# Performance work log

Hardware: AMD Instinct MI355X
Metric: run time of the kernel (lower is better)

Reference implementation:

```python
import jax, jax.numpy as jnp
import numpy as np

NUM_HEADS = 16

def setup_inputs() -> dict:
    key = jax.random.key(0)
    ks = jax.random.split(key, 9)
    E = 1024
    T, B = 2048, 2
    s = E ** -0.5
    return {
        "query": jax.random.normal(ks[0], (T, B, E), dtype=jnp.float32),
        "Wq": jax.random.normal(ks[1], (E, E), dtype=jnp.float32) * s,
        "bq": jax.random.normal(ks[2], (E,), dtype=jnp.float32) * 0.02,
        "Wk": jax.random.normal(ks[3], (E, E), dtype=jnp.float32) * s,
        "bk": jax.random.normal(ks[4], (E,), dtype=jnp.float32) * 0.02,
        "Wv": jax.random.normal(ks[5], (E, E), dtype=jnp.float32) * s,
        "bv": jax.random.normal(ks[6], (E,), dtype=jnp.float32) * 0.02,
        "Wo": jax.random.normal(ks[7], (E, E), dtype=jnp.float32) * s,
        "bo": jax.random.normal(ks[8], (E,), dtype=jnp.float32) * 0.02,
    }

def reference(query, Wq, bq, Wk, bk, Wv, bv, Wo, bo):
    # query: [T, B, E] (seq-first, fairseq/ESM layout)
    T, B, E = query.shape
    H = NUM_HEADS
    D = E // H
    scaling = D ** -0.5
    # projections (eqx Linear: x @ W.T + b); note k/v also come from `query` (self-attention)
    q = (query @ Wq.T + bq) * scaling
    k = query @ Wk.T + bk
    v = query @ Wv.T + bv
    # [T, B, E] -> [B*H, T, D]
    q = q.reshape(T, B * H, D).transpose(1, 0, 2)
    k = k.reshape(T, B * H, D).transpose(1, 0, 2)
    v = v.reshape(T, B * H, D).transpose(1, 0, 2)
    # full score matrix [B*H, T, T], softmax in fp32 (as in original)
    scores = jnp.einsum('ntd,nsd->nts', q, k)
    attn_w = jax.nn.softmax(scores.astype(jnp.float32), axis=-1)
    attn = jnp.einsum('nts,nsd->ntd', attn_w.astype(v.dtype), v)
    # [B*H, T, D] -> [T, B, E]
    attn = attn.transpose(1, 0, 2).reshape(T, B, E)
    return attn @ Wo.T + bo
```

## Files before the change

### kernel.cpp

```cpp
#include <hip/hip_runtime.h>
#include <hip/hip_bf16.h>


typedef __attribute__((ext_vector_type(8))) short short8;
typedef __attribute__((ext_vector_type(4))) float f32x4;
typedef __attribute__((ext_vector_type(16))) float f32x16;
typedef __attribute__((ext_vector_type(4))) unsigned u32x4;

#define T_DIM 2048
#define B_DIM 2
#define E_DIM 1024
#define H_DIM 16
#define D_DIM 64
#define M_ROWS (T_DIM * B_DIM)
#define QKV_N (3 * E_DIM)
#define HEAD_ELEMS (32 * 2048 * 64)
#define LOG2E 1.44269504088896340736f

__device__ __forceinline__ unsigned short f2bf(float f) {
    unsigned u = __builtin_bit_cast(unsigned, f);
    unsigned r = (u + 0x7fffu + ((u >> 16) & 1u)) >> 16;
    return (unsigned short)r;
}

__device__ __forceinline__ float bf2f(unsigned short s) {
    unsigned u = ((unsigned)s) << 16;
    return __builtin_bit_cast(float, u);
}

__device__ __forceinline__ unsigned cvt_pk_bf16(float lo, float hi) {
    unsigned d;
    asm("v_cvt_pk_bf16_f32 %0, %1, %2" : "=v"(d) : "v"(lo), "v"(hi));
    return d;
}

__device__ __forceinline__ void gload_lds16(const void* g, void* l) {
    __builtin_amdgcn_global_load_lds(
        (const __attribute__((address_space(1))) void*)g,
        (__attribute__((address_space(3))) void*)l, 16, 0, 0);
}

__device__ __forceinline__ f32x16 mfma32(short8 a, short8 b, f32x16 c) {
    return __builtin_amdgcn_mfma_f32_32x32x16_bf16(a, b, c, 0, 0, 0);
}

__global__ __launch_bounds__(256) void cast_all(
    const float* __restrict__ X,
    const float* __restrict__ Wq, const float* __restrict__ Wk,
    const float* __restrict__ Wv, const float* __restrict__ Wo,
    unsigned short* __restrict__ Xbf,
    unsigned short* __restrict__ Wcat,
    unsigned short* __restrict__ Wobf)
{
    int idx = blockIdx.x * 256 + threadIdx.x;
    size_t base = (size_t)idx * 8;
    int row = (int)(base >> 10);
    int col = (int)(base & 1023);
    const float* src;
    unsigned short* dst;
    float scale = 1.0f;
    if (row < 4096) {
        src = X + base;
        dst = Xbf + base;
    } else if (row < 7168) {
        int wrow = row - 4096;
        if (wrow < 1024)      { src = Wq + ((size_t)wrow << 10) + col; scale = 0.125f * LOG2E; }
        else if (wrow < 2048) { src = Wk + ((size_t)(wrow - 1024) << 10) + col; }
        else                  { src = Wv + ((size_t)(wrow - 2048) << 10) + col; }
        dst = Wcat + ((size_t)wrow << 10) + col;
    } else {
        int wrow = row - 7168;
        src = Wo + ((size_t)wrow << 10) + col;
        dst = Wobf + ((size_t)wrow << 10) + col;
    }
    float4 f0 = *(const float4*)src;
    float4 f1 = *(const float4*)(src + 4);
    short8 r;
    r[0] = (short)f2bf(f0.x * scale);
    r[1] = (short)f2bf(f0.y * scale);
    r[2] = (short)f2bf(f0.z * scale);
    r[3] = (short)f2bf(f0.w * scale);
    r[4] = (short)f2bf(f1.x * scale);
    r[5] = (short)f2bf(f1.y * scale);
    r[6] = (short)f2bf(f1.z * scale);
    r[7] = (short)f2bf(f1.w * scale);
    *(short8*)dst = r;
}

__global__ __launch_bounds__(256) void bias_fuse(
    const float* __restrict__ bq, const float* __restrict__ bk,
    const float* __restrict__ bv, float* __restrict__ biasq)
{
    int i = blockIdx.x * 256 + threadIdx.x;
    if (i < 1024)       biasq[i] = 0.125f * LOG2E * bq[i];
    else if (i < 2048)  biasq[i] = bk[i - 1024];
    else if (i < 3072)  biasq[i] = bv[i - 2048];
}

template <int MODE>
__global__ __launch_bounds__(256) void gemm_bt(
    const unsigned short* __restrict__ A,
    const unsigned short* __restrict__ B,
    const float* __restrict__ bias,
    void* __restrict__ outp,
    int M, int N, int K)
{
    __shared__ alignas(16) unsigned short As[2][128 * 32];
    __shared__ alignas(16) unsigned short Bs[2][128 * 32];
    const int tid = threadIdx.x;
    const int wave = tid >> 6, lane = tid & 63;
    const int lr = lane & 15, lg = lane >> 4;
    const int nbx = N >> 7;
    const int bx = blockIdx.x % nbx, by = blockIdx.x / nbx;
    const int wr = wave >> 1, wc = wave & 1;

    f32x4 acc[4][4] = {};

    auto stage = [&](int buf, int kt) {
#pragma unroll
        for (int pass = 0; pass < 2; ++pass) {
            int c = pass * 256 + wave * 64 + lane;
            int row = c >> 2, kc = c & 3;
            gload_lds16(A + (size_t)(by * 128 + row) * K + kt + kc * 8,
                        (char*)&As[buf][0] + c * 16);
            gload_lds16(B + (size_t)(bx * 128 + row) * K + kt + kc * 8,
                        (char*)&Bs[buf][0] + c * 16);
        }
    };

    const int NK = K >> 5;
    stage(0, 0);
    for (int ki = 0; ki < NK; ++ki) {
        const int buf = ki & 1;
        if (ki < NK - 1) {
            stage(buf ^ 1, (ki + 1) * 32);
            asm volatile("s_waitcnt vmcnt(4)" ::: "memory");
        } else {
            asm volatile("s_waitcnt vmcnt(0)" ::: "memory");
        }
        __builtin_amdgcn_s_barrier();
        __builtin_amdgcn_sched_barrier(0);

        short8 af[4], bf[4];
#pragma unroll
        for (int m = 0; m < 4; ++m)
            af[m] = *(const short8*)&As[buf][(wr * 64 + m * 16 + lr) * 32 + lg * 8];
#pragma unroll
        for (int n = 0; n < 4; ++n)
            bf[n] = *(const short8*)&Bs[buf][(wc * 64 + n * 16 + lr) * 32 + lg * 8];
        __builtin_amdgcn_s_setprio(1);
#pragma unroll
        for (int m = 0; m < 4; ++m)
#pragma unroll
            for (int n = 0; n < 4; ++n)
                acc[m][n] = __builtin_amdgcn_mfma_f32_16x16x32_bf16(af[m], bf[n], acc[m][n], 0, 0, 0);
        __builtin_amdgcn_s_setprio(0);

        asm volatile("s_waitcnt lgkmcnt(0)" ::: "memory");
        __builtin_amdgcn_sched_barrier(0);
        __builtin_amdgcn_s_barrier();
    }

    const int gcol0 = bx * 128 + wc * 64;
    const int grow0 = by * 128 + wr * 64;
    if (MODE == 0) {
        unsigned short* qb = (unsigned short*)outp;
#pragma unroll
        for (int m = 0; m < 4; ++m) {
#pragma unroll
            for (int n = 0; n < 4; ++n) {
                int col = gcol0 + n * 16 + lr;
                float bsv = bias[col];
                int which = col >> 10;
                int e = col & 1023;
                int h = e >> 6, d = e & 63;
                if (which < 2) {
                    unsigned short* bufb = qb + (size_t)which * HEAD_ELEMS;
#pragma unroll
                    for (int j = 0; j < 4; ++j) {
                        int r = grow0 + m * 16 + lg * 4 + j;
                        int t = r >> 1, b = r & 1;
                        int bh = b * 16 + h;
                        bufb[((size_t)bh * 2048 + t) * 64 + d] = f2bf(acc[m][n][j] + bsv);
                    }
                } else {
                    unsigned* vT32 = (unsigned*)(qb + (size_t)2 * HEAD_ELEMS);
                    int t0 = (grow0 + m * 16 + lg * 4) >> 1;
                    int dwidx = t0 >> 1;
                    int dwp = (dwidx & ~6) | ((dwidx & 2) << 1) | ((dwidx & 4) >> 1);
                    unsigned w0 = (unsigned)f2bf(acc[m][n][0] + bsv) |
                                  ((unsigned)f2bf(acc[m][n][2] + bsv) << 16);
                    unsigned w1 = (unsigned)f2bf(acc[m][n][1] + bsv) |
                                  ((unsigned)f2bf(acc[m][n][3] + bsv) << 16);
                    vT32[(size_t)(h * 64 + d) * 1024 + dwp] = w0;
                    vT32[(size_t)((16 + h) * 64 + d) * 1024 + dwp] = w1;
                }
            }
        }
    } else {
        float* O = (float*)outp;
#pragma unroll
        for (int m = 0; m < 4; ++m) {
#pragma unroll
            for (int n = 0; n < 4; ++n) {
                int col = gcol0 + n * 16 + lr;
                float bsv = bias[col];
#pragma unroll
                for (int j = 0; j < 4; ++j) {
                    int r = grow0 + m * 16 + lg * 4 + j;
                    O[(size_t)r * N + col] = acc[m][n][j] + bsv;
                }
            }
        }
    }
}

struct AttnCtx {
    const unsigned short* kh;
    const unsigned short* vh;
    int tid, ql, hi;
};

template<bool DO_PV, bool DO_STAGE>
__device__ __forceinline__ void attn_step(
    const AttnCtx& cx, int kt_next,
    const char* Kb, const char* Vprv,
    char* Kst, char* Vst,
    const short8 (&qv)[4],
    const short8 (&paP)[4], short8 (&paC)[4],
    f32x16 (&accO)[2], float& lrun)
{
    const int tid = cx.tid, ql = cx.ql, hi = cx.hi;
    if constexpr (DO_STAGE) {
#pragma unroll
        for (int p = 0; p < 2; ++p) {
            int c = p * 256 + tid;
            int row = c >> 3;
            int sxb = ((c & 7) * 16) ^ ((row & 7) << 4);
            gload_lds16(cx.kh + (size_t)(kt_next + row) * 64 + (sxb >> 1), Kst + c * 16);
        }
#pragma unroll
        for (int p = 0; p < 2; ++p) {
            int c = p * 256 + tid;
            int d = c >> 3;
            int sxb = ((c & 7) * 16) ^ ((d & 7) << 4);
            gload_lds16(cx.vh + (size_t)d * 2048 + kt_next + (sxb >> 1), Vst + c * 16);
        }
        asm volatile("s_waitcnt vmcnt(4)" ::: "memory");
    } else {
        asm volatile("s_waitcnt vmcnt(0)" ::: "memory");
    }
    __builtin_amdgcn_s_barrier();
    __builtin_amdgcn_sched_barrier(0);

    f32x16 st[2] = {};
    __builtin_amdgcn_s_setprio(1);
#pragma unroll
    for (int m = 0; m < 2; ++m) {
        int krow = m * 32 + ql;
#pragma unroll
        for (int c = 0; c < 4; ++c) {
            int bo = (krow * 128 + c * 32 + hi * 16) ^ ((krow & 7) << 4);
            short8 ka = *(const short8*)(Kb + bo);
            st[m] = mfma32(ka, qv[c], st[m]);
        }
    }
    if constexpr (DO_PV) {
#pragma unroll
        for (int n = 0; n < 2; ++n) {
            int d = n * 32 + ql;
#pragma unroll
            for (int kc = 0; kc < 4; ++kc) {
                int bo = (d * 128 + kc * 32 + hi * 16) ^ ((d & 7) << 4);
                short8 va = *(const short8*)(Vprv + bo);
                accO[n] = mfma32(va, paP[kc], accO[n]);
            }
        }
    }
    __builtin_amdgcn_s_setprio(0);
    __builtin_amdgcn_sched_barrier(0);

    float rs0 = 0.f, rs1 = 0.f, rs2 = 0.f, rs3 = 0.f;
#pragma unroll
    for (int m = 0; m < 2; ++m) {
#pragma unroll
        for (int r = 0; r < 16; r += 4) {
            float e0 = __builtin_amdgcn_exp2f(st[m][r + 0]);
            float e1 = __builtin_amdgcn_exp2f(st[m][r + 1]);
            float e2 = __builtin_amdgcn_exp2f(st[m][r + 2]);
            float e3 = __builtin_amdgcn_exp2f(st[m][r + 3]);
            st[m][r + 0] = e0; st[m][r + 1] = e1;
            st[m][r + 2] = e2; st[m][r + 3] = e3;
            rs0 += e0; rs1 += e1; rs2 += e2; rs3 += e3;
        }
    }
    lrun += (rs0 + rs1) + (rs2 + rs3);

#pragma unroll
    for (int kc = 0; kc < 4; ++kc) {
        int m = kc >> 1, b8 = (kc & 1) * 8;
        u32x4 u;
        u[0] = cvt_pk_bf16(st[m][b8 + 0], st[m][b8 + 1]);
        u[1] = cvt_pk_bf16(st[m][b8 + 2], st[m][b8 + 3]);
        u[2] = cvt_pk_bf16(st[m][b8 + 4], st[m][b8 + 5]);
        u[3] = cvt_pk_bf16(st[m][b8 + 6], st[m][b8 + 7]);
        paC[kc] = __builtin_bit_cast(short8, u);
    }

    asm volatile("s_waitcnt lgkmcnt(0)" ::: "memory");
    __builtin_amdgcn_sched_barrier(0);
    __builtin_amdgcn_s_barrier();
}

__global__ __launch_bounds__(256, 4) void attn_fwd(
    const unsigned short* __restrict__ q,
    const unsigned short* __restrict__ k,
    const unsigned short* __restrict__ vT,
    unsigned short* __restrict__ o0,
    unsigned short* __restrict__ o1,
    float* __restrict__ lsum)
{
    __shared__ alignas(16) unsigned short Ks[2][64 * 64];
    __shared__ alignas(16) unsigned short Vs[3][64 * 64];
    const int tid = threadIdx.x, wv = tid >> 6, l = tid & 63;
    const int ql = l & 31, hi = l >> 5;
    const int lid = blockIdx.x;
    const int xcd = lid & 7, slot = lid >> 3;
    const int bh = xcd * 4 + (slot >> 5);
    const int sub = slot & 31;
    const int q0 = (sub >> 1) * 128;
    const int half = sub & 1;
    const int kv0 = half * 1024;
    const unsigned short* qh = q + (size_t)bh * (2048 * 64);
    AttnCtx cx;
    cx.kh = k + (size_t)bh * (2048 * 64);
    cx.vh = vT + (size_t)bh * (64 * 2048);
    cx.tid = tid; cx.ql = ql; cx.hi = hi;

    char* K0 = (char*)&Ks[0][0];
    char* K1 = (char*)&Ks[1][0];
    char* V0 = (char*)&Vs[0][0];
    char* V1 = (char*)&Vs[1][0];
    char* V2 = (char*)&Vs[2][0];
    auto VB = [&](int i) -> char* { return i == 0 ? V0 : (i == 1 ? V1 : V2); };

    const int qrow = q0 + wv * 32 + ql;
    short8 qv[4];
#pragma unroll
    for (int c = 0; c < 4; ++c)
        qv[c] = *(const short8*)&qh[(size_t)qrow * 64 + c * 16 + hi * 8];

    f32x16 accO[2] = {};
    float lrun = 0.0f;
    short8 paA[4], paB[4];

    {
#pragma unroll
        for (int p = 0; p < 2; ++p) {
            int c = p * 256 + tid;
            int row = c >> 3;
            int sxb = ((c & 7) * 16) ^ ((row & 7) << 4);
            gload_lds16(cx.kh + (size_t)(kv0 + row) * 64 + (sxb >> 1), K0 + c * 16);
        }
#pragma unroll
        for (int p = 0; p < 2; ++p) {
            int c = p * 256 + tid;
            int d = c >> 3;
            int sxb = ((c & 7) * 16) ^ ((d & 7) << 4);
            gload_lds16(cx.vh + (size_t)d * 2048 + kv0 + (sxb >> 1), V0 + c * 16);
        }
    }

    int vp = 2, vn = 1;
    int vc = 0;
    auto rot = [&]() { vp = vc; vc = vn; vn = (vn == 2) ? 0 : vn + 1; };

    attn_step<false, true>(cx, kv0 + 64, K0, nullptr, K1, VB(vn), qv, paB, paA, accO, lrun);
    rot();
    for (int t = 1; t < 15; t += 2) {
        attn_step<true, true>(cx, kv0 + (t + 1) * 64, K1, VB(vp), K0, VB(vn),
                              qv, paA, paB, accO, lrun);
        rot();
        attn_step<true, true>(cx, kv0 + (t + 2) * 64, K0, VB(vp), K1, VB(vn),
                              qv, paB, paA, accO, lrun);
        rot();
    }
    attn_step<true, false>(cx, 0, K1, VB(vp), nullptr, nullptr, qv, paA, paB, accO, lrun);
#pragma unroll
    for (int n = 0; n < 2; ++n) {
        int d = n * 32 + ql;
#pragma unroll
        for (int kc = 0; kc < 4; ++kc) {
            int bo = (d * 128 + kc * 32 + hi * 16) ^ ((d & 7) << 4);
            short8 va = *(const short8*)(V0 + bo);
            accO[n] = mfma32(va, paB[kc], accO[n]);
        }
    }

    const float lh = lrun + __shfl_xor(lrun, 32);
    if (hi == 0)
        lsum[half * 65536 + bh * 2048 + qrow] = lh;
    unsigned short* outb = half ? o1 : o0;
    const int b = bh >> 4, h = bh & 15;
    const int orow = qrow * 2 + b;
#pragma unroll
    for (int n = 0; n < 2; ++n)
#pragma unroll
        for (int rq = 0; rq < 4; ++rq) {
            uint2 u;
            u.x = cvt_pk_bf16(accO[n][rq * 4 + 0], accO[n][rq * 4 + 1]);
            u.y = cvt_pk_bf16(accO[n][rq * 4 + 2], accO[n][rq * 4 + 3]);
            *(uint2*)&outb[(size_t)orow * 1024 + h * 64 + n * 32 + rq * 8 + hi * 4] = u;
        }
}

__global__ __launch_bounds__(256) void merge_attn(
    const unsigned short* __restrict__ o1,
    const float* __restrict__ lsum,
    unsigned short* __restrict__ o0)
{
    int idx = blockIdx.x * 256 + threadIdx.x;
    size_t base = (size_t)idx * 8;
    int r = (int)(base >> 10), cb = (int)(base & 1023);
    int t = r >> 1, b = r & 1, h = cb >> 6;
    int bh = b * 16 + h;
    float l0 = lsum[bh * 2048 + t];
    float l1 = lsum[65536 + bh * 2048 + t];
    float inv = 1.0f / (l0 + l1);
    short8 x = *(const short8*)(o0 + base);
    short8 y = *(const short8*)(o1 + base);
    u32x4 u;
#pragma unroll
    for (int j = 0; j < 4; ++j) {
        float f0 = (bf2f((unsigned short)x[2*j])   + bf2f((unsigned short)y[2*j]))   * inv;
        float f1 = (bf2f((unsigned short)x[2*j+1]) + bf2f((unsigned short)y[2*j+1])) * inv;
        u[j] = cvt_pk_bf16(f0, f1);
    }
    *(short8*)(o0 + base) = __builtin_bit_cast(short8, u);
}

extern "C" void kernel_launch(void* const* d_in, const int* in_sizes, int n_in,
                              void* d_out, int out_size, void* d_ws, size_t ws_size,
                              hipStream_t stream) {
    const float* X  = (const float*)d_in[0];
    const float* Wq = (const float*)d_in[1];
    const float* bq = (const float*)d_in[2];
    const float* Wk = (const float*)d_in[3];
    const float* bk = (const float*)d_in[4];
    const float* Wv = (const float*)d_in[5];
    const float* bv = (const float*)d_in[6];
    const float* Wo = (const float*)d_in[7];
    const float* bo = (const float*)d_in[8];
    float* out = (float*)d_out;

    char* ws = (char*)d_ws;
    if (ws_size < ((size_t)49 << 20)) return;
    unsigned short* Xbf   = (unsigned short*)(ws);
    unsigned short* Wcat  = (unsigned short*)(ws + ((size_t)8  << 20));
    unsigned short* Wobf  = (unsigned short*)(ws + ((size_t)14 << 20));
    unsigned short* qb    = (unsigned short*)(ws + ((size_t)16 << 20));
    unsigned short* ab    = (unsigned short*)(ws + ((size_t)40 << 20));
    float*          biasq = (float*)(ws + ((size_t)48 << 20));
    unsigned short* kb  = qb + (size_t)HEAD_ELEMS;
    unsigned short* vTb = qb + (size_t)2 * HEAD_ELEMS;
    unsigned short* o1   = Xbf;
    float*          lsum = (float*)Wcat;

    cast_all<<<4096, 256, 0, stream>>>(X, Wq, Wk, Wv, Wo, Xbf, Wcat, Wobf);
    bias_fuse<<<12, 256, 0, stream>>>(bq, bk, bv, biasq);
    gemm_bt<0><<<dim3((M_ROWS / 128) * (QKV_N / 128)), 256, 0, stream>>>(
        Xbf, Wcat, biasq, (void*)qb, M_ROWS, QKV_N, E_DIM);
    attn_fwd<<<dim3(32 * 16 * 2), 256, 0, stream>>>(qb, kb, vTb, ab, o1, lsum);
    merge_attn<<<2048, 256, 0, stream>>>(o1, lsum, ab);
    gemm_bt<1><<<dim3((M_ROWS / 128) * (E_DIM / 128)), 256, 0, stream>>>(
        ab, Wobf, bo, (void*)out, M_ROWS, E_DIM, E_DIM);
}
```

Measured before the change: 127.6 us.

## Process two query tiles per wave and drop split-KV merge kernel

The attention kernel now gives each wave 64 query rows as two 32-row tiles. Both tiles share the K fragments loaded from LDS and the V reads in the PV step, which halves LDS traffic per query. The KV split into two halves is removed: each block walks the full 2048-key sequence, normalises by the row sum itself and writes the final output. This removes the merge_attn kernel and its partial-output and lsum round trip through memory. In exchange the grid shrinks from 1024 to 256 blocks, launch bounds allow fewer blocks per CU, and register pressure roughly doubles, which can cut occupancy and latency hiding.

```diff
diff --git a/kernel.cpp b/kernel.cpp
--- a/kernel.cpp
+++ b/kernel.cpp
@@ -21,11 +21,6 @@
     unsigned u = __builtin_bit_cast(unsigned, f);
     unsigned r = (u + 0x7fffu + ((u >> 16) & 1u)) >> 16;
     return (unsigned short)r;
-}
-
-__device__ __forceinline__ float bf2f(unsigned short s) {
-    unsigned u = ((unsigned)s) << 16;
-    return __builtin_bit_cast(float, u);
 }
 
 __device__ __forceinline__ unsigned cvt_pk_bf16(float lo, float hi) {
@@ -226,9 +221,11 @@
     const AttnCtx& cx, int kt_next,
     const char* Kb, const char* Vprv,
     char* Kst, char* Vst,
-    const short8 (&qv)[4],
-    const short8 (&paP)[4], short8 (&paC)[4],
-    f32x16 (&accO)[2], float& lrun)
+    const short8 (&qv0)[4], const short8 (&qv1)[4],
+    const short8 (&paP0)[4], const short8 (&paP1)[4],
+    short8 (&paC0)[4], short8 (&paC1)[4],
+    f32x16 (&accO0)[2], f32x16 (&accO1)[2],
+    float& lrun0, float& lrun1)
 {
     const int tid = cx.tid, ql = cx.ql, hi = cx.hi;
     if constexpr (DO_STAGE) {
@@ -253,18 +250,24 @@
     __builtin_amdgcn_s_barrier();
     __builtin_amdgcn_sched_barrier(0);
 
-    f32x16 st[2] = {};
-    __builtin_amdgcn_s_setprio(1);
+    short8 ka[8];
 #pragma unroll
     for (int m = 0; m < 2; ++m) {
         int krow = m * 32 + ql;
 #pragma unroll
         for (int c = 0; c < 4; ++c) {
             int bo = (krow * 128 + c * 32 + hi * 16) ^ ((krow & 7) << 4);
-            short8 ka = *(const short8*)(Kb + bo);
-            st[m] = mfma32(ka, qv[c], st[m]);
-        }
-    }
+            ka[m * 4 + c] = *(const short8*)(Kb + bo);
+        }
+    }
+
+    f32x16 st0[2] = {}, st1[2] = {};
+    __builtin_amdgcn_s_setprio(1);
+#pragma unroll
+    for (int m = 0; m < 2; ++m)
+#pragma unroll
+        for (int c = 0; c < 4; ++c)
+            st0[m] = mfma32(ka[m * 4 + c], qv0[c], st0[m]);
     if constexpr (DO_PV) {
 #pragma unroll
         for (int n = 0; n < 2; ++n) {
@@ -273,38 +276,69 @@
             for (int kc = 0; kc < 4; ++kc) {
                 int bo = (d * 128 + kc * 32 + hi * 16) ^ ((d & 7) << 4);
                 short8 va = *(const short8*)(Vprv + bo);
-                accO[n] = mfma32(va, paP[kc], accO[n]);
-            }
-        }
-    }
+                accO0[n] = mfma32(va, paP0[kc], accO0[n]);
+                accO1[n] = mfma32(va, paP1[kc], accO1[n]);
+            }
+        }
+    }
+#pragma unroll
+    for (int m = 0; m < 2; ++m)
+#pragma unroll
+        for (int c = 0; c < 4; ++c)
+            st1[m] = mfma32(ka[m * 4 + c], qv1[c], st1[m]);
     __builtin_amdgcn_s_setprio(0);
-    __builtin_amdgcn_sched_barrier(0);
-
-    float rs0 = 0.f, rs1 = 0.f, rs2 = 0.f, rs3 = 0.f;
-#pragma unroll
-    for (int m = 0; m < 2; ++m) {
-#pragma unroll
-        for (int r = 0; r < 16; r += 4) {
-            float e0 = __builtin_amdgcn_exp2f(st[m][r + 0]);
-            float e1 = __builtin_amdgcn_exp2f(st[m][r + 1]);
-            float e2 = __builtin_amdgcn_exp2f(st[m][r + 2]);
-            float e3 = __builtin_amdgcn_exp2f(st[m][r + 3]);
-            st[m][r + 0] = e0; st[m][r + 1] = e1;
-            st[m][r + 2] = e2; st[m][r + 3] = e3;
-            rs0 += e0; rs1 += e1; rs2 += e2; rs3 += e3;
-        }
-    }
-    lrun += (rs0 + rs1) + (rs2 + rs3);
-
-#pragma unroll
-    for (int kc = 0; kc < 4; ++kc) {
-        int m = kc >> 1, b8 = (kc & 1) * 8;
-        u32x4 u;
-        u[0] = cvt_pk_bf16(st[m][b8 + 0], st[m][b8 + 1]);
-        u[1] = cvt_pk_bf16(st[m][b8 + 2], st[m][b8 + 3]);
-        u[2] = cvt_pk_bf16(st[m][b8 + 4], st[m][b8 + 5]);
-        u[3] = cvt_pk_bf16(st[m][b8 + 6], st[m][b8 + 7]);
-        paC[kc] = __builtin_bit_cast(short8, u);
+
+    {
+        float rs0 = 0.f, rs1 = 0.f, rs2 = 0.f, rs3 = 0.f;
+#pragma unroll
+        for (int m = 0; m < 2; ++m)
+#pragma unroll
+            for (int r = 0; r < 16; r += 4) {
+                float e0 = __builtin_amdgcn_exp2f(st0[m][r + 0]);
+                float e1 = __builtin_amdgcn_exp2f(st0[m][r + 1]);
+                float e2 = __builtin_amdgcn_exp2f(st0[m][r + 2]);
+                float e3 = __builtin_amdgcn_exp2f(st0[m][r + 3]);
+                st0[m][r + 0] = e0; st0[m][r + 1] = e1;
+                st0[m][r + 2] = e2; st0[m][r + 3] = e3;
+                rs0 += e0; rs1 += e1; rs2 += e2; rs3 += e3;
+            }
+        lrun0 += (rs0 + rs1) + (rs2 + rs3);
+#pragma unroll
+        for (int kc = 0; kc < 4; ++kc) {
+            int m = kc >> 1, b8 = (kc & 1) * 8;
+            u32x4 u;
+            u[0] = cvt_pk_bf16(st0[m][b8 + 0], st0[m][b8 + 1]);
+            u[1] = cvt_pk_bf16(st0[m][b8 + 2], st0[m][b8 + 3]);
+            u[2] = cvt_pk_bf16(st0[m][b8 + 4], st0[m][b8 + 5]);
+            u[3] = cvt_pk_bf16(st0[m][b8 + 6], st0[m][b8 + 7]);
+            paC0[kc] = __builtin_bit_cast(short8, u);
+        }
+    }
+    {
+        float rs0 = 0.f, rs1 = 0.f, rs2 = 0.f, rs3 = 0.f;
+#pragma unroll
+        for (int m = 0; m < 2; ++m)
+#pragma unroll
+            for (int r = 0; r < 16; r += 4) {
+                float e0 = __builtin_amdgcn_exp2f(st1[m][r + 0]);
+                float e1 = __builtin_amdgcn_exp2f(st1[m][r + 1]);
+                float e2 = __builtin_amdgcn_exp2f(st1[m][r + 2]);
+                float e3 = __builtin_amdgcn_exp2f(st1[m][r + 3]);
+                st1[m][r + 0] = e0; st1[m][r + 1] = e1;
+                st1[m][r + 2] = e2; st1[m][r + 3] = e3;
+                rs0 += e0; rs1 += e1; rs2 += e2; rs3 += e3;
+            }
+        lrun1 += (rs0 + rs1) + (rs2 + rs3);
+#pragma unroll
+        for (int kc = 0; kc < 4; ++kc) {
+            int m = kc >> 1, b8 = (kc & 1) * 8;
+            u32x4 u;
+            u[0] = cvt_pk_bf16(st1[m][b8 + 0], st1[m][b8 + 1]);
+            u[1] = cvt_pk_bf16(st1[m][b8 + 2], st1[m][b8 + 3]);
+            u[2] = cvt_pk_bf16(st1[m][b8 + 4], st1[m][b8 + 5]);
+            u[3] = cvt_pk_bf16(st1[m][b8 + 6], st1[m][b8 + 7]);
+            paC1[kc] = __builtin_bit_cast(short8, u);
+        }
     }
 
     asm volatile("s_waitcnt lgkmcnt(0)" ::: "memory");
@@ -312,13 +346,11 @@
     __builtin_amdgcn_s_barrier();
 }
 
-__global__ __launch_bounds__(256, 4) void attn_fwd(
+__global__ __launch_bounds__(256, 2) void attn_fwd(
     const unsigned short* __restrict__ q,
     const unsigned short* __restrict__ k,
     const unsigned short* __restrict__ vT,
-    unsigned short* __restrict__ o0,
-    unsigned short* __restrict__ o1,
-    float* __restrict__ lsum)
+    unsigned short* __restrict__ outb)
 {
     __shared__ alignas(16) unsigned short Ks[2][64 * 64];
     __shared__ alignas(16) unsigned short Vs[3][64 * 64];
@@ -326,11 +358,8 @@
     const int ql = l & 31, hi = l >> 5;
     const int lid = blockIdx.x;
     const int xcd = lid & 7, slot = lid >> 3;
-    const int bh = xcd * 4 + (slot >> 5);
-    const int sub = slot & 31;
-    const int q0 = (sub >> 1) * 128;
-    const int half = sub & 1;
-    const int kv0 = half * 1024;
+    const int bh = xcd * 4 + (slot >> 3);
+    const int q0 = (slot & 7) * 256;
     const unsigned short* qh = q + (size_t)bh * (2048 * 64);
     AttnCtx cx;
     cx.kh = k + (size_t)bh * (2048 * 64);
@@ -344,15 +373,17 @@
     char* V2 = (char*)&Vs[2][0];
     auto VB = [&](int i) -> char* { return i == 0 ? V0 : (i == 1 ? V1 : V2); };
 
-    const int qrow = q0 + wv * 32 + ql;
-    short8 qv[4];
-#pragma unroll
-    for (int c = 0; c < 4; ++c)
-        qv[c] = *(const short8*)&qh[(size_t)qrow * 64 + c * 16 + hi * 8];
-
-    f32x16 accO[2] = {};
-    float lrun = 0.0f;
-    short8 paA[4], paB[4];
+    const int qrow0 = q0 + wv * 64 + ql;
+    short8 qv0[4], qv1[4];
+#pragma unroll
+    for (int c = 0; c < 4; ++c) {
+        qv0[c] = *(const short8*)&qh[(size_t)qrow0 * 64 + c * 16 + hi * 8];
+        qv1[c] = *(const short8*)&qh[(size_t)(qrow0 + 32) * 64 + c * 16 + hi * 8];
+    }
+
+    f32x16 accO0[2] = {}, accO1[2] = {};
+    float lrun0 = 0.0f, lrun1 = 0.0f;
+    short8 paA0[4], paA1[4], paB0[4], paB1[4];
 
     {
 #pragma unroll
@@ -360,83 +391,69 @@
             int c = p * 256 + tid;
             int row = c >> 3;
             int sxb = ((c & 7) * 16) ^ ((row & 7) << 4);
-            gload_lds16(cx.kh + (size_t)(kv0 + row) * 64 + (sxb >> 1), K0 + c * 16);
+            gload_lds16(cx.kh + (size_t)row * 64 + (sxb >> 1), K0 + c * 16);
         }
 #pragma unroll
         for (int p = 0; p < 2; ++p) {
             int c = p * 256 + tid;
             int d = c >> 3;
             int sxb = ((c & 7) * 16) ^ ((d & 7) << 4);
-            gload_lds16(cx.vh + (size_t)d * 2048 + kv0 + (sxb >> 1), V0 + c * 16);
-        }
-    }
-
-    int vp = 2, vn = 1;
-    int vc = 0;
+            gload_lds16(cx.vh + (size_t)d * 2048 + (sxb >> 1), V0 + c * 16);
+        }
+    }
+
+    int vp = 2, vc = 0, vn = 1;
     auto rot = [&]() { vp = vc; vc = vn; vn = (vn == 2) ? 0 : vn + 1; };
 
-    attn_step<false, true>(cx, kv0 + 64, K0, nullptr, K1, VB(vn), qv, paB, paA, accO, lrun);
+    attn_step<false, true>(cx, 64, K0, nullptr, K1, VB(vn),
+                           qv0, qv1, paB0, paB1, paA0, paA1,
+                           accO0, accO1, lrun0, lrun1);
     rot();
-    for (int t = 1; t < 15; t += 2) {
-        attn_step<true, true>(cx, kv0 + (t + 1) * 64, K1, VB(vp), K0, VB(vn),
-                              qv, paA, paB, accO, lrun);
+    for (int t = 1; t < 31; t += 2) {
+        attn_step<true, true>(cx, (t + 1) * 64, K1, VB(vp), K0, VB(vn),
+                              qv0, qv1, paA0, paA1, paB0, paB1,
+                              accO0, accO1, lrun0, lrun1);
         rot();
-        attn_step<true, true>(cx, kv0 + (t + 2) * 64, K0, VB(vp), K1, VB(vn),
-                              qv, paB, paA, accO, lrun);
+        attn_step<true, true>(cx, (t + 2) * 64, K0, VB(vp), K1, VB(vn),
+                              qv0, qv1, paB0, paB1, paA0, paA1,
+                              accO0, accO1, lrun0, lrun1);
         rot();
     }
-    attn_step<true, false>(cx, 0, K1, VB(vp), nullptr, nullptr, qv, paA, paB, accO, lrun);
-#pragma unroll
-    for (int n = 0; n < 2; ++n) {
-        int d = n * 32 + ql;
-#pragma unroll
-        for (int kc = 0; kc < 4; ++kc) {
-            int bo = (d * 128 + kc * 32 + hi * 16) ^ ((d & 7) << 4);
-            short8 va = *(const short8*)(V0 + bo);
-            accO[n] = mfma32(va, paB[kc], accO[n]);
-        }
-    }
-
-    const float lh = lrun + __shfl_xor(lrun, 32);
-    if (hi == 0)
-        lsum[half * 65536 + bh * 2048 + qrow] = lh;
-    unsigned short* outb = half ? o1 : o0;
+    attn_step<true, false>(cx, 0, K1, VB(vp), nullptr, nullptr,
+                           qv0, qv1, paA0, paA1, paB0, paB1,
+                           accO0, accO1, lrun0, lrun1);
+    {
+        const char* Vlast = VB(vc);
+#pragma unroll
+        for (int n = 0; n < 2; ++n) {
+            int d = n * 32 + ql;
+#pragma unroll
+            for (int kc = 0; kc < 4; ++kc) {
+                int bo = (d * 128 + kc * 32 + hi * 16) ^ ((d & 7) << 4);
+                short8 va = *(const short8*)(Vlast + bo);
+                accO0[n] = mfma32(va, paB0[kc], accO0[n]);
+                accO1[n] = mfma32(va, paB1[kc], accO1[n]);
+            }
+        }
+    }
+
+    const float inv0 = 1.0f / (lrun0 + __shfl_xor(lrun0, 32));
+    const float inv1 = 1.0f / (lrun1 + __shfl_xor(lrun1, 32));
     const int b = bh >> 4, h = bh & 15;
-    const int orow = qrow * 2 + b;
+    const int orow0 = qrow0 * 2 + b;
 #pragma unroll
     for (int n = 0; n < 2; ++n)
 #pragma unroll
         for (int rq = 0; rq < 4; ++rq) {
             uint2 u;
-            u.x = cvt_pk_bf16(accO[n][rq * 4 + 0], accO[n][rq * 4 + 1]);
-            u.y = cvt_pk_bf16(accO[n][rq * 4 + 2], accO[n][rq * 4 + 3]);
-            *(uint2*)&outb[(size_t)orow * 1024 + h * 64 + n * 32 + rq * 8 + hi * 4] = u;
-        }
-}
-
-__global__ __launch_bounds__(256) void merge_attn(
-    const unsigned short* __restrict__ o1,
-    const float* __restrict__ lsum,
-    unsigned short* __restrict__ o0)
-{
-    int idx = blockIdx.x * 256 + threadIdx.x;
-    size_t base = (size_t)idx * 8;
-    int r = (int)(base >> 10), cb = (int)(base & 1023);
-    int t = r >> 1, b = r & 1, h = cb >> 6;
-    int bh = b * 16 + h;
-    float l0 = lsum[bh * 2048 + t];
-    float l1 = lsum[65536 + bh * 2048 + t];
-    float inv = 1.0f / (l0 + l1);
-    short8 x = *(const short8*)(o0 + base);
-    short8 y = *(const short8*)(o1 + base);
-    u32x4 u;
-#pragma unroll
-    for (int j = 0; j < 4; ++j) {
-        float f0 = (bf2f((unsigned short)x[2*j])   + bf2f((unsigned short)y[2*j]))   * inv;
-        float f1 = (bf2f((unsigned short)x[2*j+1]) + bf2f((unsigned short)y[2*j+1])) * inv;
-        u[j] = cvt_pk_bf16(f0, f1);
-    }
-    *(short8*)(o0 + base) = __builtin_bit_cast(short8, u);
+            u.x = cvt_pk_bf16(accO0[n][rq * 4 + 0] * inv0, accO0[n][rq * 4 + 1] * inv0);
+            u.y = cvt_pk_bf16(accO0[n][rq * 4 + 2] * inv0, accO0[n][rq * 4 + 3] * inv0);
+            *(uint2*)&outb[(size_t)orow0 * 1024 + h * 64 + n * 32 + rq * 8 + hi * 4] = u;
+            uint2 w;
+            w.x = cvt_pk_bf16(accO1[n][rq * 4 + 0] * inv1, accO1[n][rq * 4 + 1] * inv1);
+            w.y = cvt_pk_bf16(accO1[n][rq * 4 + 2] * inv1, accO1[n][rq * 4 + 3] * inv1);
+            *(uint2*)&outb[(size_t)(orow0 + 64) * 1024 + h * 64 + n * 32 + rq * 8 + hi * 4] = w;
+        }
 }
 
 extern "C" void kernel_launch(void* const* d_in, const int* in_sizes, int n_in,
@@ -463,15 +480,12 @@
     float*          biasq = (float*)(ws + ((size_t)48 << 20));
     unsigned short* kb  = qb + (size_t)HEAD_ELEMS;
     unsigned short* vTb = qb + (size_t)2 * HEAD_ELEMS;
-    unsigned short* o1   = Xbf;
-    float*          lsum = (float*)Wcat;
 
     cast_all<<<4096, 256, 0, stream>>>(X, Wq, Wk, Wv, Wo, Xbf, Wcat, Wobf);
     bias_fuse<<<12, 256, 0, stream>>>(bq, bk, bv, biasq);
     gemm_bt<0><<<dim3((M_ROWS / 128) * (QKV_N / 128)), 256, 0, stream>>>(
         Xbf, Wcat, biasq, (void*)qb, M_ROWS, QKV_N, E_DIM);
-    attn_fwd<<<dim3(32 * 16 * 2), 256, 0, stream>>>(qb, kb, vTb, ab, o1, lsum);
-    merge_attn<<<2048, 256, 0, stream>>>(o1, lsum, ab);
+    attn_fwd<<<dim3(32 * 8), 256, 0, stream>>>(qb, kb, vTb, ab);
     gemm_bt<1><<<dim3((M_ROWS / 128) * (E_DIM / 128)), 256, 0, stream>>>(
         ab, Wobf, bo, (void*)out, M_ROWS, E_DIM, E_DIM);
 }
```

New measurement: 126.8 us. Within noise of the previous version (-0.6%).
